# Performance work log

Hardware: AMD Instinct MI355X
Metric: run time of the kernel (lower is better)

The kernel has to match this reference:

```python
import jax, jax.numpy as jnp
import numpy as np

NUM_BINS = 36
MIN_ACTIVATION = 0.1
PENALTY_WEIGHT = 1.0


def setup_inputs() -> dict:
    key = jax.random.key(0)
    k1, k2 = jax.random.split(key)
    mask = jax.random.uniform(k1, (64, 1, 640, 640), dtype=jnp.float32)
    bbox = jax.random.uniform(k2, (64, 4), dtype=jnp.float32)
    return {"mask": mask, "bbox": bbox}


def reference(mask, bbox):
    B, _, H, W = mask.shape
    nb = NUM_BINS
    # pixel-space bbox centers
    cx = bbox[:, 0] * W  # (B,)
    cy = bbox[:, 1] * H  # (B,)
    x = jnp.arange(W, dtype=jnp.float32)
    y = jnp.arange(H, dtype=jnp.float32)
    # (B, H, W) offsets from each sample's center
    dx = x[None, None, :] - cx[:, None, None]
    dy = y[None, :, None] - cy[:, None, None]
    angles = jnp.arctan2(dy, dx)  # (B, H, W) in [-pi, pi]
    binf = (angles + jnp.pi) / (2.0 * jnp.pi) * nb
    bins = jnp.clip(binf.astype(jnp.int32), 0, nb - 1)  # (B, H, W)
    # fused per-(sample, bin) segment mean via a single scatter-add pass
    seg = (bins + jnp.arange(B, dtype=jnp.int32)[:, None, None] * nb).reshape(-1)
    m = mask[:, 0].reshape(-1)
    sums = jax.ops.segment_sum(m, seg, num_segments=B * nb)
    cnts = jax.ops.segment_sum(jnp.ones_like(m), seg, num_segments=B * nb)
    act = jnp.where(cnts > 0, sums / jnp.maximum(cnts, 1.0), 0.0).reshape(B, nb)
    under = (act < MIN_ACTIVATION).astype(jnp.float32)
    penalty_per_sample = under.sum(axis=1) / nb
    return PENALTY_WEIGHT * penalty_per_sample.mean()
```

## Files before the change

kernel.cpp:

```cpp
#include <hip/hip_runtime.h>
#include <math.h>

#define NB 36
#define W 640
#define H 640
#define NSAMP 64
#define RPB 40
#define BPS 16
#define NBLK (NSAMP * BPS)
#define FIX_SCALE 4194304.0f
#define INV_FIX (1.0f/4194304.0f)
#define CNT_SHIFT 44
#define SUM_MASK ((1ull << CNT_SHIFT) - 1)
#define AMB 1e-6

typedef float __attribute__((ext_vector_type(4))) f32x4;

__device__ __forceinline__ f32x4 ldnt(const float* p) {
    return __builtin_nontemporal_load((const f32x4*)p);
}

__device__ __constant__ double COT[36] = {
    0.0,
    5.6712818196177095,  2.7474774194546223,  1.7320508075688773,
    1.1917535925942100,  0.8390996311772800,  0.5773502691896258,
    0.3639702342662024,  0.1763269807084650,  0.0,
    -0.1763269807084650, -0.3639702342662024, -0.5773502691896258,
    -0.8390996311772800, -1.1917535925942100, -1.7320508075688773,
    -2.7474774194546223, -5.6712818196177095,
    0.0,
    5.6712818196177095,  2.7474774194546223,  1.7320508075688773,
    1.1917535925942100,  0.8390996311772800,  0.5773502691896258,
    0.3639702342662024,  0.1763269807084650,  0.0,
    -0.1763269807084650, -0.3639702342662024, -0.5773502691896258,
    -0.8390996311772800, -1.1917535925942100, -1.7320508075688773,
    -2.7474774194546223, -5.6712818196177095
};

__device__ __forceinline__ int bin_slow(int x, int y, double cxd, double cyd) {
    const double PI_D    = 3.141592653589793;
    const double TWOPI_D = 6.283185307179586;
    double t  = (atan2((double)y - cyd, (double)x - cxd) + PI_D) / TWOPI_D;
    double bd = t * 36.0;
    int k = (int)bd;
    k = k < 0 ? 0 : k;
    return k > NB - 1 ? NB - 1 : k;
}

#define SCAN_STEP(x, ctrl, rmask)                                             \
    x += (unsigned)__builtin_amdgcn_update_dpp(0, (int)(x), (ctrl), (rmask),  \
                                               0xf, false)

__global__ __launch_bounds__(256) void acl_main(const float* __restrict__ mask,
                                                const float* __restrict__ bbox,
                                                unsigned long long* __restrict__ ws) {
    __shared__ int A_l[RPB][18];
    __shared__ int sgn_l[RPB];
    __shared__ __align__(16) unsigned srow[8][768];
    __shared__ unsigned long long lbin[NB];

    const int tid = threadIdx.x;
    const int b   = blockIdx.x >> 4;
    const int rg  = blockIdx.x & (BPS - 1);
    const int y0  = rg * RPB;

    if (tid < NB) lbin[tid] = 0ull;
    if (tid < RPB) A_l[tid][17] = W - 1;

    const int wid = tid >> 6, lane = tid & 63;
    const float* wb = mask + (size_t)b * (W * H) + (size_t)(y0 + wid * 10) * W;
    const f32x4 z4 = 0.0f;
    const int o0 = lane * 4, o1 = lane * 4 + 256, o2 = lane * 4 + 512;

    f32x4 cA0 = ldnt(wb + o0),     cA1 = ldnt(wb + o1);
    f32x4 cA2 = (lane < 32) ? ldnt(wb + o2) : z4;
    f32x4 cB0 = ldnt(wb + W + o0), cB1 = ldnt(wb + W + o1);
    f32x4 cB2 = (lane < 32) ? ldnt(wb + W + o2) : z4;
    f32x4 dA0 = ldnt(wb + 2*W + o0), dA1 = ldnt(wb + 2*W + o1);
    f32x4 dA2 = (lane < 32) ? ldnt(wb + 2*W + o2) : z4;
    f32x4 dB0 = ldnt(wb + 3*W + o0), dB1 = ldnt(wb + 3*W + o1);
    f32x4 dB2 = (lane < 32) ? ldnt(wb + 3*W + o2) : z4;

    const double cxd = (double)bbox[b * 4 + 0] * 640.0;
    const double cyd = (double)bbox[b * 4 + 1] * 640.0;

    for (int task = tid; task < RPB * 17; task += 256) {
        const int rl = task / 17, mi = task % 17;
        const int y  = y0 + rl;
        const double dy = (double)y - cyd;
        int i, a;
        if (dy == 0.0) {
            if (mi == 0) sgn_l[rl] = 0;
            i = mi;
            a = (mi == 0) ? ((int)ceil(cxd) - 1) : (W - 1);
        } else {
            const bool dp = (dy > 0.0);
            if (mi == 0) sgn_l[rl] = dp ? 1 : -1;
            const int m = dp ? (19 + mi) : (1 + mi);
            double x = cxd + dy * COT[m];
            x = fmin(fmax(x, -2.0), 642.0);
            double g  = x + 2.0;
            int    gi = (int)g;
            double fr = g - (double)gi;
            int v = dp ? (gi - 2)
                       : (gi - 1);
            if (fr < AMB || fr > 1.0 - AMB) {
                int xa = (int)(x + 2.5) - 2;
                if (xa >= 0 && xa <= W - 1) {
                    int kb = bin_slow(xa, y, cxd, cyd);
                    if (dp) v = (kb >= m) ? xa : xa - 1;
                    else    v = (kb >= m) ? xa : xa + 1;
                }
            }
            if (dp) { i = 16 - mi; a = v; }
            else    { i = mi;      a = v - 1; }
        }
        a = a < -1 ? -1 : (a > W - 1 ? W - 1 : a);
        A_l[rl][i] = a;
    }
    __syncthreads();

    unsigned long long accPs = 0ull, accNs = 0ull;
    unsigned accPc = 0u, accNc = 0u;

    #pragma unroll
    for (int j = 0; j < 5; j++) {
        const int rl0 = wid * 10 + 2 * j;
        f32x4 nA0 = z4, nA1 = z4, nA2 = z4, nB0 = z4, nB1 = z4, nB2 = z4;
        if (j < 3) {
            const float* pa = wb + (size_t)(2 * j + 4) * W;
            const float* pb = wb + (size_t)(2 * j + 5) * W;
            nA0 = ldnt(pa + o0); nA1 = ldnt(pa + o1);
            nA2 = (lane < 32) ? ldnt(pa + o2) : z4;
            nB0 = ldnt(pb + o0); nB1 = ldnt(pb + o1);
            nB2 = (lane < 32) ? ldnt(pb + o2) : z4;
        }

        unsigned carryA = 0u, carryB = 0u;
        #pragma unroll
        for (int s = 0; s < 3; s++) {
            const f32x4 va = (s == 0) ? cA0 : (s == 1) ? cA1 : cA2;
            const f32x4 vb = (s == 0) ? cB0 : (s == 1) ? cB1 : cB2;
            const unsigned qa0 = __float2uint_rn(va.x * FIX_SCALE);
            const unsigned qa1 = __float2uint_rn(va.y * FIX_SCALE);
            const unsigned qa2 = __float2uint_rn(va.z * FIX_SCALE);
            const unsigned qa3 = __float2uint_rn(va.w * FIX_SCALE);
            const unsigned qb0 = __float2uint_rn(vb.x * FIX_SCALE);
            const unsigned qb1 = __float2uint_rn(vb.y * FIX_SCALE);
            const unsigned qb2 = __float2uint_rn(vb.z * FIX_SCALE);
            const unsigned qb3 = __float2uint_rn(vb.w * FIX_SCALE);
            const unsigned pa0 = qa0, pa1 = pa0 + qa1, pa2 = pa1 + qa2, pa3 = pa2 + qa3;
            const unsigned pb0 = qb0, pb1 = pb0 + qb1, pb2 = pb1 + qb2, pb3 = pb2 + qb3;

            unsigned xa = pa3, xb = pb3;
            SCAN_STEP(xa, 0x111, 0xf); SCAN_STEP(xb, 0x111, 0xf);
            SCAN_STEP(xa, 0x112, 0xf); SCAN_STEP(xb, 0x112, 0xf);
            SCAN_STEP(xa, 0x114, 0xf); SCAN_STEP(xb, 0x114, 0xf);
            SCAN_STEP(xa, 0x118, 0xf); SCAN_STEP(xb, 0x118, 0xf);
            SCAN_STEP(xa, 0x142, 0xa); SCAN_STEP(xb, 0x142, 0xa);
            SCAN_STEP(xa, 0x143, 0xc); SCAN_STEP(xb, 0x143, 0xc);

            const unsigned baA = carryA + (xa - pa3);
            const unsigned baB = carryB + (xb - pb3);
            uint4 wa, wbv;
            wa.x  = baA + pa0; wa.y  = baA + pa1; wa.z  = baA + pa2; wa.w  = baA + pa3;
            wbv.x = baB + pb0; wbv.y = baB + pb1; wbv.z = baB + pb2; wbv.w = baB + pb3;
            *((uint4*)&srow[wid][s * 256 + lane * 4])     = wa;
            *((uint4*)&srow[wid + 4][s * 256 + lane * 4]) = wbv;
            carryA += (unsigned)__builtin_amdgcn_readlane((int)xa, 63);
            carryB += (unsigned)__builtin_amdgcn_readlane((int)xb, 63);
        }

        if (lane < 18) {
            #pragma unroll
            for (int r = 0; r < 2; r++) {
                const int rl = rl0 + r;
                const int slab = wid + 4 * r;
                const int aR = A_l[rl][lane];
                const int aL = (lane == 0) ? -1 : A_l[rl][lane - 1];
                const int cnt = aR - aL;
                if (cnt > 0) {
                    const unsigned sR = srow[slab][aR];
                    const unsigned sL = (aL >= 0) ? srow[slab][aL] : 0u;
                    const unsigned seg = sR - sL;
                    const int sg = sgn_l[rl];
                    if (sg > 0)      { accPc += (unsigned)cnt; accPs += seg; }
                    else if (sg < 0) { accNc += (unsigned)cnt; accNs += seg; }
                    else atomicAdd(&lbin[(lane == 0) ? 35 : 18],
                                   ((unsigned long long)cnt << CNT_SHIFT)
                                   + (unsigned long long)seg);
                }
            }
        }
        cA0 = dA0; cA1 = dA1; cA2 = dA2; cB0 = dB0; cB1 = dB1; cB2 = dB2;
        dA0 = nA0; dA1 = nA1; dA2 = nA2; dB0 = nB0; dB1 = nB1; dB2 = nB2;
    }

    if (lane < 18) {
        if (accPc) atomicAdd(&lbin[35 - lane],
                             ((unsigned long long)accPc << CNT_SHIFT) + accPs);
        if (accNc) atomicAdd(&lbin[lane],
                             ((unsigned long long)accNc << CNT_SHIFT) + accNs);
    }
    __syncthreads();
    if (tid < NB)
        ws[(size_t)tid * NBLK + blockIdx.x] = lbin[tid];
}

__global__ __launch_bounds__(256) void acl_final(const unsigned long long* __restrict__ ws,
                                                 float* __restrict__ out) {
    __shared__ unsigned nund[256];
    __shared__ float s[NSAMP];
    const int tid = threadIdx.x;
    const int b = tid & 63, q = tid >> 6;
    unsigned cu = 0;
    #pragma unroll
    for (int kk = 0; kk < 9; kk++) {
        const int k = q * 9 + kk;
        const unsigned long long* base = ws + (size_t)k * NBLK + (size_t)b * BPS;
        unsigned long long t0 = 0ull, t1 = 0ull;
        #pragma unroll
        for (int g = 0; g < BPS; g += 2) {
            t0 += base[g];
            t1 += base[g + 1];
        }
        const unsigned long long tot = t0 + t1;
        const unsigned long long cnt = tot >> CNT_SHIFT;
        const float sum = (float)(tot & SUM_MASK) * INV_FIX;
        const float act = (cnt != 0ull) ? (sum / (float)cnt) : 0.0f;
        if (act < 0.1f) cu++;
    }
    nund[tid] = cu;
    __syncthreads();
    if (tid < NSAMP) {
        const unsigned n = nund[tid] + nund[64 + tid] + nund[128 + tid] + nund[192 + tid];
        s[tid] = (float)n / 36.0f;
    }
    __syncthreads();
    if (tid == 0) {
        float acc = 0.0f;
        for (int i = 0; i < NSAMP; i++) acc += s[i];
        out[0] = acc / 64.0f;
    }
}

extern "C" void kernel_launch(void* const* d_in, const int* in_sizes, int n_in,
                              void* d_out, int out_size, void* d_ws, size_t ws_size,
                              hipStream_t stream) {
    const float* mask = (const float*)d_in[0];
    const float* bbox = (const float*)d_in[1];
    unsigned long long* ws = (unsigned long long*)d_ws;

    acl_main<<<dim3(NBLK), dim3(256), 0, stream>>>(mask, bbox, ws);
    acl_final<<<dim3(1), dim3(256), 0, stream>>>(ws, (float*)d_out);
}
```

Before: 34.06 us.

## Fuse final reduction into main kernel via last-block counter; DPP neighbor exchange

Merges the final reduction kernel into the main kernel. A global atomic counter picks the last finishing block, and that block reads every per-block partial and writes the output. The per-row segment lookup now reads only the right boundary from LDS and gets the left neighbor's value through a DPP lane shift, saving one LDS load per row. To do this the launch now adds a memset and a tiny setptr kernel that stores the output pointer in the workspace. So the launch count does not really drop, and the code also contains a redundant duplicated tail block with a dead store.

```diff
diff --git a/kernel.cpp b/kernel.cpp
--- a/kernel.cpp
+++ b/kernel.cpp
@@ -17,7 +17,7 @@
 typedef float __attribute__((ext_vector_type(4))) f32x4;
 
 __device__ __forceinline__ f32x4 ldnt(const float* p) {
-    return __builtin_nontemporal_load((const f32x4*)p);
+    return __builtin_nontemporal_load((const f32x4*)(p));
 }
 
 __device__ __constant__ double COT[36] = {
@@ -51,13 +51,14 @@
     x += (unsigned)__builtin_amdgcn_update_dpp(0, (int)(x), (ctrl), (rmask),  \
                                                0xf, false)
 
-__global__ __launch_bounds__(256) void acl_main(const float* __restrict__ mask,
-                                                const float* __restrict__ bbox,
-                                                unsigned long long* __restrict__ ws) {
+__global__ __launch_bounds__(256) void acl_fused(const float* __restrict__ mask,
+                                                 const float* __restrict__ bbox,
+                                                 unsigned long long* __restrict__ ws) {
     __shared__ int A_l[RPB][18];
     __shared__ int sgn_l[RPB];
     __shared__ __align__(16) unsigned srow[8][768];
     __shared__ unsigned long long lbin[NB];
+    __shared__ int slast;
 
     const int tid = threadIdx.x;
     const int b   = blockIdx.x >> 4;
@@ -171,17 +172,21 @@
             carryB += (unsigned)__builtin_amdgcn_readlane((int)xb, 63);
         }
 
-        if (lane < 18) {
-            #pragma unroll
-            for (int r = 0; r < 2; r++) {
-                const int rl = rl0 + r;
-                const int slab = wid + 4 * r;
-                const int aR = A_l[rl][lane];
-                const int aL = (lane == 0) ? -1 : A_l[rl][lane - 1];
+        #pragma unroll
+        for (int r = 0; r < 2; r++) {
+            const int rl = rl0 + r;
+            const int slab = wid + 4 * r;
+            const int aR = A_l[rl][(lane < 18) ? lane : 17];
+            const int idx = aR & ~(aR >> 31);
+            const unsigned sRraw = srow[slab][idx];
+            const unsigned sR = (aR >= 0) ? sRraw : 0u;
+            const int aL =
+                __builtin_amdgcn_update_dpp(-1, aR, 0x138, 0xf, 0xf, false);
+            const unsigned sL = (unsigned)
+                __builtin_amdgcn_update_dpp(0, (int)sR, 0x138, 0xf, 0xf, false);
+            if (lane < 18) {
                 const int cnt = aR - aL;
                 if (cnt > 0) {
-                    const unsigned sR = srow[slab][aR];
-                    const unsigned sL = (aL >= 0) ? srow[slab][aL] : 0u;
                     const unsigned seg = sR - sL;
                     const int sg = sgn_l[rl];
                     if (sg > 0)      { accPc += (unsigned)cnt; accPs += seg; }
@@ -204,43 +209,64 @@
     }
     __syncthreads();
     if (tid < NB)
-        ws[(size_t)tid * NBLK + blockIdx.x] = lbin[tid];
-}
-
-__global__ __launch_bounds__(256) void acl_final(const unsigned long long* __restrict__ ws,
-                                                 float* __restrict__ out) {
+        __hip_atomic_store(&ws[(size_t)tid * NBLK + blockIdx.x], lbin[tid],
+                           __ATOMIC_RELAXED, __HIP_MEMORY_SCOPE_AGENT);
+
+    unsigned* cnt_p = (unsigned*)(ws + (size_t)NB * NBLK);
+    __syncthreads();
+    if (tid == 0) {
+        __threadfence();
+        unsigned old = atomicAdd(cnt_p, 1u);
+        slast = (old == NBLK - 1);
+    }
+    __syncthreads();
+    if (!slast) return;
+    __threadfence();
+
     __shared__ unsigned nund[256];
-    __shared__ float s[NSAMP];
-    const int tid = threadIdx.x;
-    const int b = tid & 63, q = tid >> 6;
+    const int fb = tid & 63, fq = tid >> 6;
     unsigned cu = 0;
     #pragma unroll
     for (int kk = 0; kk < 9; kk++) {
-        const int k = q * 9 + kk;
-        const unsigned long long* base = ws + (size_t)k * NBLK + (size_t)b * BPS;
-        unsigned long long t0 = 0ull, t1 = 0ull;
+        const int k = fq * 9 + kk;
+        const unsigned long long* base = ws + (size_t)k * NBLK + (size_t)fb * BPS;
+        unsigned long long tot = 0ull;
         #pragma unroll
-        for (int g = 0; g < BPS; g += 2) {
-            t0 += base[g];
-            t1 += base[g + 1];
-        }
-        const unsigned long long tot = t0 + t1;
-        const unsigned long long cnt = tot >> CNT_SHIFT;
+        for (int g = 0; g < BPS; g++)
+            tot += __hip_atomic_load(&base[g], __ATOMIC_RELAXED,
+                                     __HIP_MEMORY_SCOPE_AGENT);
+        const unsigned long long c = tot >> CNT_SHIFT;
         const float sum = (float)(tot & SUM_MASK) * INV_FIX;
-        const float act = (cnt != 0ull) ? (sum / (float)cnt) : 0.0f;
+        const float act = (c != 0ull) ? (sum / (float)c) : 0.0f;
         if (act < 0.1f) cu++;
     }
     nund[tid] = cu;
-    __syncthreads();
-    if (tid < NSAMP) {
-        const unsigned n = nund[tid] + nund[64 + tid] + nund[128 + tid] + nund[192 + tid];
-        s[tid] = (float)n / 36.0f;
-    }
     __syncthreads();
     if (tid == 0) {
         float acc = 0.0f;
-        for (int i = 0; i < NSAMP; i++) acc += s[i];
-        out[0] = acc / 64.0f;
+        for (int i = 0; i < NSAMP; i++) {
+            const unsigned n = nund[i] + nund[64 + i] + nund[128 + i] + nund[192 + i];
+            acc += (float)n / 36.0f;
+        }
+        float* out = (float*)(ws + (size_t)NB * NBLK + 1);
+        ((volatile float*)out)[0] = 0.0f;
+    }
+    if (tid == 0) {
+        float acc = 0.0f;
+        for (int i = 0; i < NSAMP; i++) {
+            const unsigned n = nund[i] + nund[64 + i] + nund[128 + i] + nund[192 + i];
+            acc += (float)n / 36.0f;
+        }
+        float** outpp = (float**)(ws + (size_t)NB * NBLK + 2);
+        float* outp = *outpp;
+        outp[0] = acc / 64.0f;
+    }
+}
+
+__global__ void acl_setptr(unsigned long long* __restrict__ ws, float* out) {
+    if (threadIdx.x == 0 && blockIdx.x == 0) {
+        float** outpp = (float**)(ws + (size_t)NB * NBLK + 2);
+        *outpp = out;
     }
 }
 
@@ -251,6 +277,7 @@
     const float* bbox = (const float*)d_in[1];
     unsigned long long* ws = (unsigned long long*)d_ws;
 
-    acl_main<<<dim3(NBLK), dim3(256), 0, stream>>>(mask, bbox, ws);
-    acl_final<<<dim3(1), dim3(256), 0, stream>>>(ws, (float*)d_out);
-}
+    hipMemsetAsync((void*)(ws + (size_t)NB * NBLK), 0, 8, stream);
+    acl_setptr<<<dim3(1), dim3(64), 0, stream>>>(ws, (float*)d_out);
+    acl_fused<<<dim3(NBLK), dim3(256), 0, stream>>>(mask, bbox, ws);
+}
```

Result: slower. 86.60 us (+154.2%).
